# Kernel optimization log

Hardware: AMD Instinct MI355X
Metric: run time of the kernel (lower is better)

## Reference

```python
import jax, jax.numpy as jnp
import numpy as np

N = 16384      # n_samples
D = 1024       # embedding_size
C = 16         # number of classes (balanced so every anchor has a positive)
MARGIN = 1.0
EPS = 1e-6


def setup_inputs() -> dict:
    rng = np.random.default_rng(0)
    labels = np.arange(N) % C
    rng.shuffle(labels)
    # positive index: same label, different sample (random within-class rotation)
    pos = np.empty(N, dtype=np.int64)
    for c in range(C):
        idx = np.nonzero(labels == c)[0]
        off = rng.integers(1, len(idx), size=len(idx))
        pos[idx] = idx[(np.arange(len(idx)) + off) % len(idx)]
    # negative index: any sample with a different label (rejection-resample on host)
    neg = rng.integers(0, N, size=N)
    while True:
        bad = labels[neg] == labels
        if not bad.any():
            break
        neg[bad] = rng.integers(0, N, size=int(bad.sum()))
    key = jax.random.key(0)
    embeddings = jax.random.normal(key, (N, D), dtype=jnp.float32)
    return {
        "embeddings": embeddings,
        "labels": jnp.asarray(labels, dtype=jnp.int64),
        "pos_idx": jnp.asarray(pos, dtype=jnp.int64),
        "neg_idx": jnp.asarray(neg, dtype=jnp.int64),
    }


def reference(embeddings, labels, pos_idx, neg_idx):
    # F.normalize(p=2, dim=1, eps=1e-6): x / max(||x||_2, eps)
    norm = jnp.sqrt(jnp.sum(embeddings * embeddings, axis=1, keepdims=True))
    e = embeddings / jnp.maximum(norm, EPS)                      # [N, D]

    def pdist(a, b):
        # F.pairwise_distance adds eps to the difference; module adds another +eps
        return jnp.sqrt(jnp.sum((a - b + EPS) ** 2, axis=1)) + EPS

    d_pos = pdist(e, e[pos_idx])                                 # [N]
    d_neg = pdist(e, e[neg_idx])                                 # [N]
    positive_loss = d_pos ** 2
    negative_loss = jnp.maximum(MARGIN - d_neg, EPS) ** 2
    total = jnp.sum(positive_loss) + jnp.sum(negative_loss)
    return total / (2.0 * N)
```

## Files before the change

kernel.cpp:

```cpp
#include <hip/hip_runtime.h>

#define NROWS 16384
#define DIM   1024
#define F4_PER_ROW 256
#define F4_PER_LANE 4
#define MARGIN_F 1.0f
#define EPS_F 1e-6f

__global__ __launch_bounds__(256) void row_loss_kernel(
    const float* __restrict__ emb,
    const int*   __restrict__ pos_idx,
    const int*   __restrict__ neg_idx,
    float*       __restrict__ losses)
{
    const int tid  = threadIdx.x;
    const int lane = tid & 63;
    const int wid  = tid >> 6;
    const int row  = blockIdx.x * 4 + wid;

    const int p = pos_idx[row];
    const int n = neg_idx[row];

    const float4* xi = (const float4*)(emb + (size_t)row * DIM);
    const float4* xp = (const float4*)(emb + (size_t)p   * DIM);
    const float4* xn = (const float4*)(emb + (size_t)n   * DIM);

    float4 a[F4_PER_LANE], b[F4_PER_LANE], c[F4_PER_LANE];
    #pragma unroll
    for (int j = 0; j < F4_PER_LANE; ++j) {
        a[j] = xi[lane + 64 * j];
        b[j] = xp[lane + 64 * j];
        c[j] = xn[lane + 64 * j];
    }

    float ni = 0.f, np_ = 0.f, nn = 0.f;
    #pragma unroll
    for (int j = 0; j < F4_PER_LANE; ++j) {
        ni  = fmaf(a[j].x, a[j].x, ni);  ni  = fmaf(a[j].y, a[j].y, ni);
        ni  = fmaf(a[j].z, a[j].z, ni);  ni  = fmaf(a[j].w, a[j].w, ni);
        np_ = fmaf(b[j].x, b[j].x, np_); np_ = fmaf(b[j].y, b[j].y, np_);
        np_ = fmaf(b[j].z, b[j].z, np_); np_ = fmaf(b[j].w, b[j].w, np_);
        nn  = fmaf(c[j].x, c[j].x, nn);  nn  = fmaf(c[j].y, c[j].y, nn);
        nn  = fmaf(c[j].z, c[j].z, nn);  nn  = fmaf(c[j].w, c[j].w, nn);
    }
    #pragma unroll
    for (int m = 1; m < 64; m <<= 1) {
        ni  += __shfl_xor(ni,  m, 64);
        np_ += __shfl_xor(np_, m, 64);
        nn  += __shfl_xor(nn,  m, 64);
    }
    const float si = 1.0f / fmaxf(sqrtf(ni),  EPS_F);
    const float sp = 1.0f / fmaxf(sqrtf(np_), EPS_F);
    const float sn = 1.0f / fmaxf(sqrtf(nn),  EPS_F);

    float sum_p = 0.f, sum_n = 0.f;
    #pragma unroll
    for (int j = 0; j < F4_PER_LANE; ++j) {
        float t;
        t = fmaf(a[j].x, si, -b[j].x * sp) + EPS_F; sum_p = fmaf(t, t, sum_p);
        t = fmaf(a[j].y, si, -b[j].y * sp) + EPS_F; sum_p = fmaf(t, t, sum_p);
        t = fmaf(a[j].z, si, -b[j].z * sp) + EPS_F; sum_p = fmaf(t, t, sum_p);
        t = fmaf(a[j].w, si, -b[j].w * sp) + EPS_F; sum_p = fmaf(t, t, sum_p);
        t = fmaf(a[j].x, si, -c[j].x * sn) + EPS_F; sum_n = fmaf(t, t, sum_n);
        t = fmaf(a[j].y, si, -c[j].y * sn) + EPS_F; sum_n = fmaf(t, t, sum_n);
        t = fmaf(a[j].z, si, -c[j].z * sn) + EPS_F; sum_n = fmaf(t, t, sum_n);
        t = fmaf(a[j].w, si, -c[j].w * sn) + EPS_F; sum_n = fmaf(t, t, sum_n);
    }
    #pragma unroll
    for (int m = 1; m < 64; m <<= 1) {
        sum_p += __shfl_xor(sum_p, m, 64);
        sum_n += __shfl_xor(sum_n, m, 64);
    }

    if (lane == 0) {
        float d_pos = sqrtf(sum_p) + EPS_F;
        float d_neg = sqrtf(sum_n) + EPS_F;
        float mq = fmaxf(MARGIN_F - d_neg, EPS_F);
        losses[row] = d_pos * d_pos + mq * mq;
    }
}

__global__ __launch_bounds__(1024) void final_reduce_kernel(
    const float* __restrict__ losses,
    float*       __restrict__ out)
{
    const int tid  = threadIdx.x;
    const int lane = tid & 63;
    const int wid  = tid >> 6;

    const float4* l4 = (const float4*)losses;
    float s = 0.0f;
    #pragma unroll
    for (int j = 0; j < 4; ++j) {
        float4 v = l4[tid + 1024 * j];
        s += v.x + v.y + v.z + v.w;
    }
    #pragma unroll
    for (int m = 1; m < 64; m <<= 1) s += __shfl_xor(s, m, 64);

    __shared__ float sm[16];
    if (lane == 0) sm[wid] = s;
    __syncthreads();
    if (tid == 0) {
        float total = 0.f;
        #pragma unroll
        for (int w = 0; w < 16; ++w) total += sm[w];
        out[0] = total / (2.0f * (float)NROWS);
    }
}

extern "C" void kernel_launch(void* const* d_in, const int* in_sizes, int n_in,
                              void* d_out, int out_size, void* d_ws, size_t ws_size,
                              hipStream_t stream) {
    const float* emb = (const float*)d_in[0];
    const int* pos = (const int*)d_in[2];
    const int* neg = (const int*)d_in[3];

    float* losses = (float*)d_ws;
    float* out    = (float*)d_out;

    row_loss_kernel<<<NROWS / 4, 256, 0, stream>>>(emb, pos, neg, losses);
    final_reduce_kernel<<<1, 1024, 0, stream>>>(losses, out);
}
```

Measured before the change: 112.6 us.

## Expand squared distance algebraically into norms, dot products and sums in one pass

Each squared distance is rewritten as a combination of row norms, dot products and element sums, so the second elementwise pass and its shuffle reduction go away and the loaded rows no longer need to stay in registers. Loads are staggered so the accumulation overlaps outstanding loads, and launch bounds request higher occupancy. Per-block partial sums replace per-row losses, which shrinks the final reduction. The expanded form can lose precision through cancellation when rows are nearly identical; it is clamped at zero before the square root.

```diff
diff --git a/kernel.cpp b/kernel.cpp
--- a/kernel.cpp
+++ b/kernel.cpp
@@ -2,16 +2,14 @@
 
 #define NROWS 16384
 #define DIM   1024
-#define F4_PER_ROW 256
-#define F4_PER_LANE 4
 #define MARGIN_F 1.0f
 #define EPS_F 1e-6f
 
-__global__ __launch_bounds__(256) void row_loss_kernel(
+__global__ __launch_bounds__(256, 8) void row_loss_kernel(
     const float* __restrict__ emb,
     const int*   __restrict__ pos_idx,
     const int*   __restrict__ neg_idx,
-    float*       __restrict__ losses)
+    float*       __restrict__ block_part)
 {
     const int tid  = threadIdx.x;
     const int lane = tid & 63;
@@ -21,92 +19,89 @@
     const int p = pos_idx[row];
     const int n = neg_idx[row];
 
-    const float4* xi = (const float4*)(emb + (size_t)row * DIM);
-    const float4* xp = (const float4*)(emb + (size_t)p   * DIM);
-    const float4* xn = (const float4*)(emb + (size_t)n   * DIM);
-
-    float4 a[F4_PER_LANE], b[F4_PER_LANE], c[F4_PER_LANE];
-    #pragma unroll
-    for (int j = 0; j < F4_PER_LANE; ++j) {
-        a[j] = xi[lane + 64 * j];
-        b[j] = xp[lane + 64 * j];
-        c[j] = xn[lane + 64 * j];
-    }
+    const float4* xi = (const float4*)(emb + (size_t)row * DIM) + lane;
+    const float4* xp = (const float4*)(emb + (size_t)p   * DIM) + lane;
+    const float4* xn = (const float4*)(emb + (size_t)n   * DIM) + lane;
 
     float ni = 0.f, np_ = 0.f, nn = 0.f;
-    #pragma unroll
-    for (int j = 0; j < F4_PER_LANE; ++j) {
-        ni  = fmaf(a[j].x, a[j].x, ni);  ni  = fmaf(a[j].y, a[j].y, ni);
-        ni  = fmaf(a[j].z, a[j].z, ni);  ni  = fmaf(a[j].w, a[j].w, ni);
-        np_ = fmaf(b[j].x, b[j].x, np_); np_ = fmaf(b[j].y, b[j].y, np_);
-        np_ = fmaf(b[j].z, b[j].z, np_); np_ = fmaf(b[j].w, b[j].w, np_);
-        nn  = fmaf(c[j].x, c[j].x, nn);  nn  = fmaf(c[j].y, c[j].y, nn);
-        nn  = fmaf(c[j].z, c[j].z, nn);  nn  = fmaf(c[j].w, c[j].w, nn);
-    }
+    float dip = 0.f, din = 0.f;
+    float sa = 0.f, sb = 0.f, sc = 0.f;
+
+    float4 a0 = xi[0],   b0 = xp[0],   c0 = xn[0];
+    float4 a1 = xi[64],  b1 = xp[64],  c1 = xn[64];
+
+    #define ACC(A,B,C)                                                                                     \
+        ni  = fmaf(A.x,A.x,ni);  ni  = fmaf(A.y,A.y,ni);  ni  = fmaf(A.z,A.z,ni);  ni  = fmaf(A.w,A.w,ni); \
+        np_ = fmaf(B.x,B.x,np_); np_ = fmaf(B.y,B.y,np_); np_ = fmaf(B.z,B.z,np_); np_ = fmaf(B.w,B.w,np_);\
+        nn  = fmaf(C.x,C.x,nn);  nn  = fmaf(C.y,C.y,nn);  nn  = fmaf(C.z,C.z,nn);  nn  = fmaf(C.w,C.w,nn); \
+        dip = fmaf(A.x,B.x,dip); dip = fmaf(A.y,B.y,dip); dip = fmaf(A.z,B.z,dip); dip = fmaf(A.w,B.w,dip);\
+        din = fmaf(A.x,C.x,din); din = fmaf(A.y,C.y,din); din = fmaf(A.z,C.z,din); din = fmaf(A.w,C.w,din);\
+        sa += (A.x + A.y) + (A.z + A.w);                                                                   \
+        sb += (B.x + B.y) + (B.z + B.w);                                                                   \
+        sc += (C.x + C.y) + (C.z + C.w);
+
+    float4 a2 = xi[128], b2 = xp[128], c2 = xn[128];
+    ACC(a0, b0, c0)
+    float4 a3 = xi[192], b3 = xp[192], c3 = xn[192];
+    ACC(a1, b1, c1)
+    ACC(a2, b2, c2)
+    ACC(a3, b3, c3)
+    #undef ACC
+
     #pragma unroll
     for (int m = 1; m < 64; m <<= 1) {
         ni  += __shfl_xor(ni,  m, 64);
         np_ += __shfl_xor(np_, m, 64);
         nn  += __shfl_xor(nn,  m, 64);
-    }
-    const float si = 1.0f / fmaxf(sqrtf(ni),  EPS_F);
-    const float sp = 1.0f / fmaxf(sqrtf(np_), EPS_F);
-    const float sn = 1.0f / fmaxf(sqrtf(nn),  EPS_F);
-
-    float sum_p = 0.f, sum_n = 0.f;
-    #pragma unroll
-    for (int j = 0; j < F4_PER_LANE; ++j) {
-        float t;
-        t = fmaf(a[j].x, si, -b[j].x * sp) + EPS_F; sum_p = fmaf(t, t, sum_p);
-        t = fmaf(a[j].y, si, -b[j].y * sp) + EPS_F; sum_p = fmaf(t, t, sum_p);
-        t = fmaf(a[j].z, si, -b[j].z * sp) + EPS_F; sum_p = fmaf(t, t, sum_p);
-        t = fmaf(a[j].w, si, -b[j].w * sp) + EPS_F; sum_p = fmaf(t, t, sum_p);
-        t = fmaf(a[j].x, si, -c[j].x * sn) + EPS_F; sum_n = fmaf(t, t, sum_n);
-        t = fmaf(a[j].y, si, -c[j].y * sn) + EPS_F; sum_n = fmaf(t, t, sum_n);
-        t = fmaf(a[j].z, si, -c[j].z * sn) + EPS_F; sum_n = fmaf(t, t, sum_n);
-        t = fmaf(a[j].w, si, -c[j].w * sn) + EPS_F; sum_n = fmaf(t, t, sum_n);
-    }
-    #pragma unroll
-    for (int m = 1; m < 64; m <<= 1) {
-        sum_p += __shfl_xor(sum_p, m, 64);
-        sum_n += __shfl_xor(sum_n, m, 64);
+        dip += __shfl_xor(dip, m, 64);
+        din += __shfl_xor(din, m, 64);
+        sa  += __shfl_xor(sa,  m, 64);
+        sb  += __shfl_xor(sb,  m, 64);
+        sc  += __shfl_xor(sc,  m, 64);
     }
 
+    __shared__ float sm[4];
     if (lane == 0) {
-        float d_pos = sqrtf(sum_p) + EPS_F;
-        float d_neg = sqrtf(sum_n) + EPS_F;
-        float mq = fmaxf(MARGIN_F - d_neg, EPS_F);
-        losses[row] = d_pos * d_pos + mq * mq;
+        const float si = 1.0f / fmaxf(sqrtf(ni),  EPS_F);
+        const float sp = 1.0f / fmaxf(sqrtf(np_), EPS_F);
+        const float sn = 1.0f / fmaxf(sqrtf(nn),  EPS_F);
+        const float de2 = (float)DIM * EPS_F * EPS_F;
+
+        float sum_p = fmaf(si * si, ni, fmaf(sp * sp, np_, -2.f * si * sp * dip))
+                    + 2.f * EPS_F * (si * sa - sp * sb) + de2;
+        float sum_n = fmaf(si * si, ni, fmaf(sn * sn, nn, -2.f * si * sn * din))
+                    + 2.f * EPS_F * (si * sa - sn * sc) + de2;
+
+        float d_pos = sqrtf(fmaxf(sum_p, 0.f)) + EPS_F;
+        float d_neg = sqrtf(fmaxf(sum_n, 0.f)) + EPS_F;
+        float mq    = fmaxf(MARGIN_F - d_neg, EPS_F);
+        sm[wid] = fmaf(d_pos, d_pos, mq * mq);
     }
+    __syncthreads();
+    if (tid == 0)
+        block_part[blockIdx.x] = (sm[0] + sm[1]) + (sm[2] + sm[3]);
 }
 
-__global__ __launch_bounds__(1024) void final_reduce_kernel(
-    const float* __restrict__ losses,
+__global__ __launch_bounds__(256) void final_reduce_kernel(
+    const float* __restrict__ part,
     float*       __restrict__ out)
 {
-    const int tid  = threadIdx.x;
-    const int lane = tid & 63;
-    const int wid  = tid >> 6;
-
-    const float4* l4 = (const float4*)losses;
-    float s = 0.0f;
+    const int tid = threadIdx.x;
+    const float4* p4 = (const float4*)part;
+    float s = 0.f;
     #pragma unroll
     for (int j = 0; j < 4; ++j) {
-        float4 v = l4[tid + 1024 * j];
-        s += v.x + v.y + v.z + v.w;
+        float4 v = p4[tid + 256 * j];
+        s += (v.x + v.y) + (v.z + v.w);
     }
     #pragma unroll
     for (int m = 1; m < 64; m <<= 1) s += __shfl_xor(s, m, 64);
 
-    __shared__ float sm[16];
-    if (lane == 0) sm[wid] = s;
+    __shared__ float sm[4];
+    if ((tid & 63) == 0) sm[tid >> 6] = s;
     __syncthreads();
-    if (tid == 0) {
-        float total = 0.f;
-        #pragma unroll
-        for (int w = 0; w < 16; ++w) total += sm[w];
-        out[0] = total / (2.0f * (float)NROWS);
-    }
+    if (tid == 0)
+        out[0] = ((sm[0] + sm[1]) + (sm[2] + sm[3])) * (1.0f / (2.0f * (float)NROWS));
 }
 
 extern "C" void kernel_launch(void* const* d_in, const int* in_sizes, int n_in,
@@ -116,9 +111,9 @@
     const int* pos = (const int*)d_in[2];
     const int* neg = (const int*)d_in[3];
 
-    float* losses = (float*)d_ws;
-    float* out    = (float*)d_out;
+    float* parts = (float*)d_ws;
+    float* out   = (float*)d_out;
 
-    row_loss_kernel<<<NROWS / 4, 256, 0, stream>>>(emb, pos, neg, losses);
-    final_reduce_kernel<<<1, 1024, 0, stream>>>(losses, out);
+    row_loss_kernel<<<NROWS / 4, 256, 0, stream>>>(emb, pos, neg, parts);
+    final_reduce_kernel<<<1, 256, 0, stream>>>(parts, out);
 }
```

Result: slower. 116.1 us (+3.1%).
